# Optimization experiments

Measured on AMD Instinct MI355X. Metric: run time of the kernel, lower is better.

## Reference

```python
import jax, jax.numpy as jnp
import numpy as np

NUM_HEADS = 8
EMBED_DIM = 512


def _attention(q, k, v, mask=None):
    # q,k,v: [batch, heads, Lq, d] / [batch, heads, Lk, d]
    s = jnp.einsum('bhqd,bhkd->bhqk', q, k)
    if mask is not None:
        s = jnp.where(mask, jnp.asarray(-1000.0, s.dtype), s)
    p = jax.nn.softmax(s, axis=-1)
    return jnp.einsum('bhqk,bhkd->bhqd', p, v)


def _t_mask(T, H):
    # True where attention is DISALLOWED (query frame t_q < key frame t_k)
    tq = jnp.arange(T)[:, None]
    tk = jnp.arange(T)[None, :]
    blocked = tq < tk  # [T, T]
    m = jnp.repeat(jnp.repeat(blocked, H, axis=0), H, axis=1)  # [T*H, T*H]
    return m


def setup_inputs() -> dict:
    key = jax.random.key(0)
    ks = jax.random.split(key, 10)
    B, T, H, W, E = 4, 4, 28, 28, EMBED_DIM
    N = T * H * W
    s_in = (2.0 / (E + 3 * E)) ** 0.5  # xavier-ish
    s_sq = (1.0 / E) ** 0.5
    return {
        'x': jax.random.normal(ks[0], (B, N, E), dtype=jnp.float32),
        'in_proj_weight': jax.random.normal(ks[1], (3 * E, E), dtype=jnp.float32) * s_in,
        'in_proj_bias': jnp.zeros((3 * E,), dtype=jnp.float32),
        'out_proj_w': jax.random.normal(ks[2], (E, E), dtype=jnp.float32) * s_sq,
        'out_proj_b': jnp.zeros((E,), dtype=jnp.float32),
        'in_proj_weight_t': jax.random.normal(ks[3], (E, E), dtype=jnp.float32) * s_sq,
        'in_proj_bias_t': jnp.zeros((E,), dtype=jnp.float32),
        'out_proj_t_w': jax.random.normal(ks[4], (E, E), dtype=jnp.float32) * s_sq,
        'out_proj_t_b': jnp.zeros((E,), dtype=jnp.float32),
        'alpha': 0.0001 * jnp.ones((E,), dtype=jnp.float32),
        'H': 28,
        'W': 28,
    }


def reference(x, in_proj_weight, in_proj_bias, out_proj_w, out_proj_b,
              in_proj_weight_t, in_proj_bias_t, out_proj_t_w, out_proj_t_b,
              alpha, H, W):
    B, N, C = x.shape
    nh = NUM_HEADS
    hc = C // nh
    T = N // (H * W)
    scale = hc ** (-0.5)

    # ---- spatial (per-frame) attention: _forward_2d ----
    qkv = x @ in_proj_weight.T + in_proj_bias            # [B, N, 3C]
    qkv = qkv.reshape(B, T, H * W, 3, nh, hc)
    qkv = qkv.transpose(3, 0, 1, 4, 2, 5).reshape(3, B * T, nh, H * W, hc)
    q, k, v = qkv[0], qkv[1], qkv[2]
    o = _attention(q * scale, k, v)                       # [B*T, nh, HW, hc]
    xs = o.transpose(0, 2, 1, 3).reshape(B, N, C)
    xs = xs @ out_proj_w.T + out_proj_b

    ks = jax.lax.stop_gradient(k)                         # detached cache
    vs = jax.lax.stop_gradient(v)

    # ---- axial temporal attention ----
    q_t = (x @ in_proj_weight_t.T + in_proj_bias_t) * scale  # [B, N, C]
    q_t = q_t.reshape(B, T, H, W, nh, hc)
    q_th = q_t.transpose(0, 3, 4, 1, 2, 5).reshape(B * W, nh, T * H, hc)
    q_tw = q_t.transpose(0, 2, 4, 1, 3, 5).reshape(B * H, nh, T * W, hc)

    k6 = ks.reshape(B, T, nh, H, W, hc)
    v6 = vs.reshape(B, T, nh, H, W, hc)
    k_th = k6.transpose(0, 4, 2, 1, 3, 5).reshape(B * W, nh, T * H, hc)
    k_tw = k6.transpose(0, 3, 2, 1, 4, 5).reshape(B * H, nh, T * W, hc)
    v_th = v6.transpose(0, 4, 2, 1, 3, 5).reshape(B * W, nh, T * H, hc)
    v_tw = v6.transpose(0, 3, 2, 1, 4, 5).reshape(B * H, nh, T * W, hc)

    o_th = _attention(q_th, k_th, v_th, _t_mask(T, H))    # [B*W, nh, T*H, hc]
    o_tw = _attention(q_tw, k_tw, v_tw, _t_mask(T, W))    # [B*H, nh, T*W, hc]

    o_th = o_th.reshape(B, W, nh, T, H, hc).transpose(0, 3, 4, 1, 2, 5).reshape(B, N, C)
    o_tw = o_tw.reshape(B, H, nh, T, W, hc).transpose(0, 3, 1, 4, 2, 5).reshape(B, N, C)

    x_t = (o_th + o_tw) @ out_proj_t_w.T + out_proj_t_b
    return xs + alpha * x_t
```

## Files before the change

kernel.cpp:

```cpp
#include <hip/hip_runtime.h>
#include <stdint.h>

#define NN   3136
#define MM   12544
#define SCALE 0.125f
#define MASKED (-30000.0f)

typedef __attribute__((ext_vector_type(8))) unsigned short ushort8;
typedef __attribute__((ext_vector_type(8))) short short8;
typedef __attribute__((ext_vector_type(4))) float floatx4;

__device__ __forceinline__ float b2f(unsigned short u) {
    union { unsigned int i; float f; } x; x.i = ((unsigned int)u) << 16; return x.f;
}
__device__ __forceinline__ unsigned short f2b(float f) {
    union { float f; unsigned int i; } x; x.f = f;
    unsigned int r = x.i + 0x7fffu + ((x.i >> 16) & 1u);
    return (unsigned short)(r >> 16);
}
__device__ __forceinline__ void load8(const void* p, size_t e, int isf32, float o[8]) {
    if (isf32) {
        const float* f = (const float*)p + e;
        #pragma unroll
        for (int i = 0; i < 8; ++i) o[i] = f[i];
    } else {
        ushort8 u = *(const ushort8*)((const unsigned short*)p + e);
        #pragma unroll
        for (int i = 0; i < 8; ++i) o[i] = b2f(u[i]);
    }
}
__device__ __forceinline__ float load1(const void* p, int e, int isf32) {
    return isf32 ? ((const float*)p)[e] : b2f(((const unsigned short*)p)[e]);
}

__global__ void detect_dtype(const void* __restrict__ x, int* __restrict__ flagp)
{
    if (threadIdx.x == 0 && blockIdx.x == 0) {
        const unsigned short* u = (const unsigned short*)x;
        int c = 0;
        for (int i = 0; i < 512; ++i) {
            const float v = b2f(u[i]);
            if (!(v == v) || fabsf(v) > 1000.0f) ++c;
        }
        *flagp = (c >= 16) ? 1 : 0;
    }
}

__global__ __launch_bounds__(256) void convert_x(
    const int* __restrict__ flagp, const float* __restrict__ x,
    unsigned short* __restrict__ xb)
{
    if (!*flagp) return;
    const size_t i = ((size_t)blockIdx.x * 256 + threadIdx.x) * 8;
    const float4 a = *(const float4*)(x + i);
    const float4 b = *(const float4*)(x + i + 4);
    ushort8 o;
    o[0] = f2b(a.x); o[1] = f2b(a.y); o[2] = f2b(a.z); o[3] = f2b(a.w);
    o[4] = f2b(b.x); o[5] = f2b(b.y); o[6] = f2b(b.z); o[7] = f2b(b.w);
    *(ushort8*)(xb + i) = o;
}

__global__ __launch_bounds__(256) void gemm_proj_mfma(
    const int* __restrict__ flagp, const void* __restrict__ x,
    const unsigned short* __restrict__ xb,
    const void* __restrict__ Wi, const void* __restrict__ bi,
    const void* __restrict__ Wt, const void* __restrict__ bt,
    unsigned short* __restrict__ qkv, unsigned short* __restrict__ qt)
{
    __shared__ unsigned short A_sh[128][40];
    __shared__ unsigned short B_sh[64][40];
    const int gid = blockIdx.x;
    const int mt = (gid >> 8) * 8 + (gid & 7);
    const int nt = (gid & 255) >> 3;
    if (mt >= 98) return;
    const int m0 = mt * 128, n0 = nt * 64;

    const int isf32 = *flagp;
    const unsigned short* A = isf32 ? xb : (const unsigned short*)x;
    const int tid = threadIdx.x, lane = tid & 63, wv = tid >> 6;
    const int lane15 = lane & 15, quad = lane >> 4;
    const int wm = wv >> 1, wn = wv & 1;

    const int ra = tid >> 1, ca = (tid & 1) * 16;
    const int rb = tid >> 2, cb = (tid & 3) * 8;
    const int nb = n0 + rb;
    const bool isWt = (nb >= 1536);

    floatx4 acc[4][2];
    #pragma unroll
    for (int i = 0; i < 4; ++i)
        #pragma unroll
        for (int j = 0; j < 2; ++j) acc[i][j] = (floatx4){0.f,0.f,0.f,0.f};

    for (int k0 = 0; k0 < 512; k0 += 32) {
        const unsigned short* ap = A + (size_t)(m0 + ra) * 512 + k0 + ca;
        *(ushort8*)&A_sh[ra][ca]     = *(const ushort8*)ap;
        *(ushort8*)&A_sh[ra][ca + 8] = *(const ushort8*)(ap + 8);
        float wvv[8];
        if (!isWt) load8(Wi, (size_t)nb * 512 + k0 + cb, isf32, wvv);
        else {
            load8(Wt, (size_t)(nb - 1536) * 512 + k0 + cb, isf32, wvv);
            #pragma unroll
            for (int u = 0; u < 8; ++u) wvv[u] *= SCALE;
        }
        #pragma unroll
        for (int u = 0; u < 8; ++u) B_sh[rb][cb + u] = f2b(wvv[u]);
        __syncthreads();

        short8 af[4], bf[2];
        #pragma unroll
        for (int i = 0; i < 4; ++i)
            af[i] = *(const short8*)&A_sh[wm * 64 + i * 16 + lane15][quad * 8];
        #pragma unroll
        for (int j = 0; j < 2; ++j)
            bf[j] = *(const short8*)&B_sh[wn * 32 + j * 16 + lane15][quad * 8];
        #pragma unroll
        for (int i = 0; i < 4; ++i)
            #pragma unroll
            for (int j = 0; j < 2; ++j)
                acc[i][j] = __builtin_amdgcn_mfma_f32_16x16x32_bf16(af[i], bf[j], acc[i][j], 0, 0, 0);
        __syncthreads();
    }

    #pragma unroll
    for (int j = 0; j < 2; ++j) {
        const int col = n0 + wn * 32 + j * 16 + lane15;
        float bias;
        unsigned short* dst;
        int stride;
        if (col < 1536) { bias = load1(bi, col, isf32); dst = qkv; stride = 1536; }
        else { bias = SCALE * load1(bt, col - 1536, isf32); dst = qt; stride = 512; }
        const int cofs = (col < 1536) ? col : (col - 1536);
        #pragma unroll
        for (int i = 0; i < 4; ++i)
            #pragma unroll
            for (int r = 0; r < 4; ++r) {
                const int m = m0 + wm * 64 + i * 16 + quad * 4 + r;
                dst[(size_t)m * stride + cofs] = f2b(acc[i][j][r] + bias);
            }
    }
}

__global__ __launch_bounds__(256) void gemm_final_mfma(
    const int* __restrict__ flagp,
    const unsigned short* __restrict__ qkv, const unsigned short* __restrict__ qt,
    const void* __restrict__ Wo, const void* __restrict__ Wto,
    const void* __restrict__ bo, const void* __restrict__ bto,
    const void* __restrict__ alp, void* __restrict__ outp)
{
    __shared__ unsigned short A_sh[128][40];
    __shared__ unsigned short B_sh[64][40];
    const int gid = blockIdx.x;
    const int mt = (gid >> 6) * 8 + (gid & 7);
    const int nt = (gid & 63) >> 3;
    if (mt >= 98) return;
    const int m0 = mt * 128, n0 = nt * 64;

    const int isf32 = *flagp;
    const int tid = threadIdx.x, lane = tid & 63, wv = tid >> 6;
    const int lane15 = lane & 15, quad = lane >> 4;
    const int wm = wv >> 1, wn = wv & 1;

    const int ra = tid >> 1, ca = (tid & 1) * 16;
    const int rb = tid >> 2, cb = (tid & 3) * 8;
    const int nb = n0 + rb;
    const float al_b = load1(alp, nb, isf32);

    floatx4 acc[4][2];
    #pragma unroll
    for (int i = 0; i < 4; ++i)
        #pragma unroll
        for (int j = 0; j < 2; ++j) acc[i][j] = (floatx4){0.f,0.f,0.f,0.f};

    for (int k0 = 0; k0 < 1024; k0 += 32) {
        const int m = m0 + ra;
        const unsigned short* ap = (k0 < 512)
            ? qkv + (size_t)m * 1536 + k0 + ca
            : qt  + (size_t)m * 512  + (k0 - 512) + ca;
        *(ushort8*)&A_sh[ra][ca]     = *(const ushort8*)ap;
        *(ushort8*)&A_sh[ra][ca + 8] = *(const ushort8*)(ap + 8);
        float wvv[8];
        if (k0 < 512) load8(Wo, (size_t)nb * 512 + k0 + cb, isf32, wvv);
        else {
            load8(Wto, (size_t)nb * 512 + (k0 - 512) + cb, isf32, wvv);
            #pragma unroll
            for (int u = 0; u < 8; ++u) wvv[u] *= al_b;
        }
        #pragma unroll
        for (int u = 0; u < 8; ++u) B_sh[rb][cb + u] = f2b(wvv[u]);
        __syncthreads();

        short8 af[4], bf[2];
        #pragma unroll
        for (int i = 0; i < 4; ++i)
            af[i] = *(const short8*)&A_sh[wm * 64 + i * 16 + lane15][quad * 8];
        #pragma unroll
        for (int j = 0; j < 2; ++j)
            bf[j] = *(const short8*)&B_sh[wn * 32 + j * 16 + lane15][quad * 8];
        #pragma unroll
        for (int i = 0; i < 4; ++i)
            #pragma unroll
            for (int j = 0; j < 2; ++j)
                acc[i][j] = __builtin_amdgcn_mfma_f32_16x16x32_bf16(af[i], bf[j], acc[i][j], 0, 0, 0);
        __syncthreads();
    }

    #pragma unroll
    for (int j = 0; j < 2; ++j) {
        const int col = n0 + wn * 32 + j * 16 + lane15;
        const float bias = load1(bo, col, isf32) + load1(alp, col, isf32) * load1(bto, col, isf32);
        #pragma unroll
        for (int i = 0; i < 4; ++i)
            #pragma unroll
            for (int r = 0; r < 4; ++r) {
                const int m = m0 + wm * 64 + i * 16 + quad * 4 + r;
                const float val = acc[i][j][r] + bias;
                const size_t idx = (size_t)m * 512 + col;
                if (isf32) ((float*)outp)[idx] = val;
                else       ((unsigned short*)outp)[idx] = f2b(val);
            }
    }
}

__global__ __launch_bounds__(256) void attn_spatial_mfma(unsigned short* __restrict__ qkv)
{
    __shared__ unsigned short K_sh[64][72];
    __shared__ unsigned short VT_sh[64][72];
    __shared__ unsigned short P_sh[4][16][72];

    const int tid = threadIdx.x, lane = tid & 63, wv = tid >> 6;
    const int lane15 = lane & 15, quad = lane >> 4;
    const int qb = blockIdx.x, head = blockIdx.y, bt = blockIdx.z;
    const int qt_idx = qb * 4 + wv;
    const bool active = (qt_idx < 49);
    const int q0 = active ? qt_idx * 16 : 0;
    const int frame0 = bt * 784;

    short8 q_lo = {0,0,0,0,0,0,0,0}, q_hi = {0,0,0,0,0,0,0,0};
    if (active) {
        const unsigned short* qp = qkv + (size_t)(frame0 + q0 + lane15) * 1536 + head * 64 + quad * 8;
        q_lo = *(const short8*)qp;
        q_hi = *(const short8*)(qp + 32);
    }

    floatx4 accO[4] = {{0.f,0.f,0.f,0.f},{0.f,0.f,0.f,0.f},{0.f,0.f,0.f,0.f},{0.f,0.f,0.f,0.f}};
    float lsum[4] = {0.f, 0.f, 0.f, 0.f};

    const int r_st = tid >> 2, c_st = (tid & 3) << 4;

    for (int kt = 0; kt < 13; ++kt) {
        __syncthreads();
        ushort8 k8a = {0,0,0,0,0,0,0,0}, k8b = {0,0,0,0,0,0,0,0};
        ushort8 v8a = {0,0,0,0,0,0,0,0}, v8b = {0,0,0,0,0,0,0,0};
        const int key = kt * 64 + r_st;
        if (key < 784) {
            const unsigned short* kp = qkv + (size_t)(frame0 + key) * 1536 + head * 64 + c_st;
            k8a = *(const ushort8*)(kp + 512);
            k8b = *(const ushort8*)(kp + 520);
            v8a = *(const ushort8*)(kp + 1024);
            v8b = *(const ushort8*)(kp + 1032);
        }
        *(ushort8*)&K_sh[r_st][c_st]     = k8a;
        *(ushort8*)&K_sh[r_st][c_st + 8] = k8b;
        #pragma unroll
        for (int u = 0; u < 8; ++u) {
            VT_sh[c_st + u][r_st]     = v8a[u];
            VT_sh[c_st + 8 + u][r_st] = v8b[u];
        }
        __syncthreads();
        if (!active) continue;

        floatx4 s[4];
        #pragma unroll
        for (int st = 0; st < 4; ++st) {
            const short8 kfl = *(const short8*)&K_sh[st * 16 + lane15][quad * 8];
            const short8 kfh = *(const short8*)&K_sh[st * 16 + lane15][32 + quad * 8];
            floatx4 a = {0.f,0.f,0.f,0.f};
            a = __builtin_amdgcn_mfma_f32_16x16x32_bf16(q_lo, kfl, a, 0, 0, 0);
            a = __builtin_amdgcn_mfma_f32_16x16x32_bf16(q_hi, kfh, a, 0, 0, 0);
            s[st] = a;
        }

        const bool tail = (kt == 12);
        #pragma unroll
        for (int st = 0; st < 4; ++st)
            #pragma unroll
            for (int r = 0; r < 4; ++r) {
                const float v = (tail && st >= 1) ? MASKED : s[st][r] * SCALE;
                const float p = __expf(v);
                lsum[r] += p;
                P_sh[wv][quad * 4 + r][st * 16 + lane15] = f2b(p);
            }

        #pragma unroll
        for (int kc = 0; kc < 2; ++kc) {
            const short8 pf = *(const short8*)&P_sh[wv][lane15][kc * 32 + quad * 8];
            #pragma unroll
            for (int nt = 0; nt < 4; ++nt) {
                const short8 vf = *(const short8*)&VT_sh[nt * 16 + lane15][kc * 32 + quad * 8];
                accO[nt] = __builtin_amdgcn_mfma_f32_16x16x32_bf16(pf, vf, accO[nt], 0, 0, 0);
            }
        }
    }

    #pragma unroll
    for (int off = 1; off < 16; off <<= 1)
        #pragma unroll
        for (int r = 0; r < 4; ++r)
            lsum[r] += __shfl_xor(lsum[r], off, 64);

    if (active) {
        #pragma unroll
        for (int nt = 0; nt < 4; ++nt)
            #pragma unroll
            for (int r = 0; r < 4; ++r) {
                const int qrow = q0 + quad * 4 + r;
                qkv[(size_t)(frame0 + qrow) * 1536 + head * 64 + nt * 16 + lane15]
                    = f2b(accO[nt][r] / lsum[r]);
            }
    }
}

__global__ __launch_bounds__(256) void attn_axial(
    const unsigned short* __restrict__ qkv, const unsigned short* __restrict__ qtu,
    const unsigned short* __restrict__ oth, unsigned short* __restrict__ outp,
    const int pass)
{
    __shared__ unsigned short K_sh[112][72];
    __shared__ unsigned short VT_sh[64][136];
    __shared__ unsigned short P_sh[4][16][136];

    const int tid = threadIdx.x, lane = tid & 63, wv = tid >> 6;
    const int lane15 = lane & 15, quad = lane >> 4;
    const int b = blockIdx.x / 28, pos = blockIdx.x % 28;
    const int head = blockIdx.y;
    const int r_st = tid >> 3, c_st = (tid & 7) << 3;

    #pragma unroll
    for (int rnd = 0; rnd < 4; ++rnd) {
        const int j = rnd * 32 + r_st;
        if (j < 112) {
            const int tk = j / 28, rk = j % 28;
            const int n_k = tk * 784 + (pass == 0 ? rk * 28 + pos : pos * 28 + rk);
            const unsigned short* kp = qkv + (size_t)(b * NN + n_k) * 1536 + 512 + head * 64 + c_st;
            const ushort8 k8 = *(const ushort8*)kp;
            const ushort8 v8 = *(const ushort8*)(kp + 512);
            *(ushort8*)&K_sh[j][c_st] = k8;
            #pragma unroll
            for (int u = 0; u < 8; ++u) VT_sh[c_st + u][j] = v8[u];
        } else {
            #pragma unroll
            for (int u = 0; u < 8; ++u) VT_sh[c_st + u][j] = 0;
        }
    }
    __syncthreads();

    for (int tile = wv; tile < 7; tile += 4) {
        const int iq = tile * 16 + lane15;
        const int tq_q = iq / 28, rq = iq % 28;
        const int n_q = tq_q * 784 + (pass == 0 ? rq * 28 + pos : pos * 28 + rq);
        const size_t qaddr = (size_t)(b * NN + n_q) * 512 + head * 64;
        const short8 q_lo = *(const short8*)(qtu + qaddr + quad * 8);
        const short8 q_hi = *(const short8*)(qtu + qaddr + 32 + quad * 8);

        floatx4 s[7];
        #pragma unroll
        for (int st = 0; st < 7; ++st) {
            const short8 kfl = *(const short8*)&K_sh[st * 16 + lane15][quad * 8];
            const short8 kfh = *(const short8*)&K_sh[st * 16 + lane15][32 + quad * 8];
            floatx4 acc = {0.f,0.f,0.f,0.f};
            acc = __builtin_amdgcn_mfma_f32_16x16x32_bf16(q_lo, kfl, acc, 0, 0, 0);
            acc = __builtin_amdgcn_mfma_f32_16x16x32_bf16(q_hi, kfh, acc, 0, 0, 0);
            s[st] = acc;
        }

        int tq_row[4];
        #pragma unroll
        for (int r = 0; r < 4; ++r) tq_row[r] = (tile * 16 + quad * 4 + r) / 28;
        float l[4] = {0.f, 0.f, 0.f, 0.f};
        #pragma unroll
        for (int st = 0; st < 7; ++st) {
            const int tk = (st * 16 + lane15) / 28;
            #pragma unroll
            for (int r = 0; r < 4; ++r) {
                const float v = (tk <= tq_row[r]) ? s[st][r] : MASKED;
                const float p = __expf(v);
                s[st][r] = p;
                l[r] += p;
            }
        }
        #pragma unroll
        for (int off = 1; off < 16; off <<= 1)
            #pragma unroll
            for (int r = 0; r < 4; ++r)
                l[r] += __shfl_xor(l[r], off, 64);

        #pragma unroll
        for (int r = 0; r < 4; ++r) {
            const int row = quad * 4 + r;
            #pragma unroll
            for (int st = 0; st < 7; ++st)
                P_sh[wv][row][st * 16 + lane15] = f2b(s[st][r]);
            P_sh[wv][row][112 + lane15] = 0;
        }

        floatx4 accO[4] = {{0.f,0.f,0.f,0.f},{0.f,0.f,0.f,0.f},{0.f,0.f,0.f,0.f},{0.f,0.f,0.f,0.f}};
        #pragma unroll
        for (int kc = 0; kc < 4; ++kc) {
            const short8 pf = *(const short8*)&P_sh[wv][lane15][kc * 32 + quad * 8];
            #pragma unroll
            for (int nt = 0; nt < 4; ++nt) {
                const short8 vf = *(const short8*)&VT_sh[nt * 16 + lane15][kc * 32 + quad * 8];
                accO[nt] = __builtin_amdgcn_mfma_f32_16x16x32_bf16(pf, vf, accO[nt], 0, 0, 0);
            }
        }

        #pragma unroll
        for (int r = 0; r < 4; ++r) {
            const int io = tile * 16 + quad * 4 + r;
            const int to = io / 28, ro = io % 28;
            const int n_o = to * 784 + (pass == 0 ? ro * 28 + pos : pos * 28 + ro);
            const size_t oaddr = (size_t)(b * NN + n_o) * 512 + head * 64;
            #pragma unroll
            for (int nt = 0; nt < 4; ++nt) {
                float o = accO[nt][r] / l[r];
                if (pass == 1) o += b2f(oth[oaddr + nt * 16 + lane15]);
                outp[oaddr + nt * 16 + lane15] = f2b(o);
            }
        }
    }
}

__global__ void fill_val(unsigned short* o, unsigned short v, int n) {
    const int i = blockIdx.x * 256 + threadIdx.x;
    if (i < n) o[i] = v;
}

extern "C" void kernel_launch(void* const* d_in, const int* in_sizes, int n_in,
                              void* d_out, int out_size, void* d_ws, size_t ws_size,
                              hipStream_t stream)
{
    const void* x   = d_in[0];
    const void* Wi  = d_in[1];
    const void* bi  = d_in[2];
    const void* Wo  = d_in[3];
    const void* bo  = d_in[4];
    const void* Wt  = d_in[5];
    const void* bt  = d_in[6];
    const void* Wto = d_in[7];
    const void* bto = d_in[8];
    const void* alp = d_in[9];

    const size_t QKV_ELEMS = (size_t)MM * 1536;
    const size_t QT_ELEMS  = (size_t)MM * 512;
    const size_t FLAG_OFF  = (QKV_ELEMS + QT_ELEMS) * 2;
    const size_t NEED      = FLAG_OFF + 256;

    if (ws_size < NEED) {
        fill_val<<<dim3((out_size + 255) / 256), dim3(256), 0, stream>>>(
            (unsigned short*)d_out, (unsigned short)0x3f80, out_size);
        return;
    }

    unsigned short* qkv = (unsigned short*)d_ws;
    unsigned short* qt  = qkv + QKV_ELEMS;
    int* flagp = (int*)((char*)d_ws + FLAG_OFF);
    unsigned short* oth = (unsigned short*)d_out;
    unsigned short* xb  = oth + (size_t)MM * 512;

    dim3 blk(256);
    detect_dtype<<<dim3(1), dim3(64), 0, stream>>>(x, flagp);
    convert_x<<<dim3(MM * 512 / (256 * 8)), blk, 0, stream>>>(flagp, (const float*)x, xb);
    gemm_proj_mfma<<<dim3(13 * 256), blk, 0, stream>>>(
        flagp, x, xb, Wi, bi, Wt, bt, qkv, qt);
    attn_spatial_mfma<<<dim3(13, 8, 16), blk, 0, stream>>>(qkv);
    attn_axial<<<dim3(112, 8), blk, 0, stream>>>(qkv, qt, nullptr, oth, 0);
    attn_axial<<<dim3(112, 8), blk, 0, stream>>>(qkv, qt, oth, qt, 1);
    gemm_final_mfma<<<dim3(13 * 64), blk, 0, stream>>>(
        flagp, qkv, qt, Wo, Wto, bo, bto, alp, d_out);
}
```

Measured before the change: 331.0 us.

## Swizzle LDS layouts for V/P tiles and remap spatial blocks per XCD

XOR-swizzles the column index of the transposed V tile and the P tile in shared memory, in both the spatial and the axial attention kernels. The goal is to cut LDS bank conflicts on the scalar transposed stores and the vector fragment reads. The spatial kernel also switches to a 1D grid whose block IDs are remapped so that all query blocks of one (frame, head) group land on the same XCD, which should improve L2 reuse of that group's K/V. The swizzles must agree exactly between writers and readers, or outputs will be wrong.

```diff
diff --git a/kernel.cpp b/kernel.cpp
--- a/kernel.cpp
+++ b/kernel.cpp
@@ -230,7 +230,13 @@
 
     const int tid = threadIdx.x, lane = tid & 63, wv = tid >> 6;
     const int lane15 = lane & 15, quad = lane >> 4;
-    const int qb = blockIdx.x, head = blockIdx.y, bt = blockIdx.z;
+
+    const int gid = blockIdx.x;
+    const int xcd = gid & 7, kk = gid >> 3;
+    const int grp = xcd * 16 + kk / 13;
+    const int qb  = kk % 13;
+    const int head = grp & 7, bt = grp >> 3;
+
     const int qt_idx = qb * 4 + wv;
     const bool active = (qt_idx < 49);
     const int q0 = active ? qt_idx * 16 : 0;
@@ -247,6 +253,8 @@
     float lsum[4] = {0.f, 0.f, 0.f, 0.f};
 
     const int r_st = tid >> 2, c_st = (tid & 3) << 4;
+    const int swzv = c_st;
+    const int swzp = (lane15 >> 2) << 4;
 
     for (int kt = 0; kt < 13; ++kt) {
         __syncthreads();
@@ -264,8 +272,8 @@
         *(ushort8*)&K_sh[r_st][c_st + 8] = k8b;
         #pragma unroll
         for (int u = 0; u < 8; ++u) {
-            VT_sh[c_st + u][r_st]     = v8a[u];
-            VT_sh[c_st + 8 + u][r_st] = v8b[u];
+            VT_sh[c_st + u][r_st ^ swzv]     = v8a[u];
+            VT_sh[c_st + 8 + u][r_st ^ swzv] = v8b[u];
         }
         __syncthreads();
         if (!active) continue;
@@ -289,15 +297,15 @@
                 const float v = (tail && st >= 1) ? MASKED : s[st][r] * SCALE;
                 const float p = __expf(v);
                 lsum[r] += p;
-                P_sh[wv][quad * 4 + r][st * 16 + lane15] = f2b(p);
+                P_sh[wv][quad * 4 + r][(st * 16 + lane15) ^ (quad << 4)] = f2b(p);
             }
 
         #pragma unroll
         for (int kc = 0; kc < 2; ++kc) {
-            const short8 pf = *(const short8*)&P_sh[wv][lane15][kc * 32 + quad * 8];
+            const short8 pf = *(const short8*)&P_sh[wv][lane15][(kc * 32 + quad * 8) ^ swzp];
             #pragma unroll
             for (int nt = 0; nt < 4; ++nt) {
-                const short8 vf = *(const short8*)&VT_sh[nt * 16 + lane15][kc * 32 + quad * 8];
+                const short8 vf = *(const short8*)&VT_sh[nt * 16 + lane15][(kc * 32 + quad * 8) ^ (nt << 4)];
                 accO[nt] = __builtin_amdgcn_mfma_f32_16x16x32_bf16(pf, vf, accO[nt], 0, 0, 0);
             }
         }
@@ -335,6 +343,7 @@
     const int b = blockIdx.x / 28, pos = blockIdx.x % 28;
     const int head = blockIdx.y;
     const int r_st = tid >> 3, c_st = (tid & 7) << 3;
+    const int swzp = (lane15 >> 2) << 4;
 
     #pragma unroll
     for (int rnd = 0; rnd < 4; ++rnd) {
@@ -347,10 +356,10 @@
             const ushort8 v8 = *(const ushort8*)(kp + 512);
             *(ushort8*)&K_sh[j][c_st] = k8;
             #pragma unroll
-            for (int u = 0; u < 8; ++u) VT_sh[c_st + u][j] = v8[u];
+            for (int u = 0; u < 8; ++u) VT_sh[c_st + u][j ^ c_st] = v8[u];
         } else {
             #pragma unroll
-            for (int u = 0; u < 8; ++u) VT_sh[c_st + u][j] = 0;
+            for (int u = 0; u < 8; ++u) VT_sh[c_st + u][j ^ c_st] = 0;
         }
     }
     __syncthreads();
@@ -400,17 +409,18 @@
             const int row = quad * 4 + r;
             #pragma unroll
             for (int st = 0; st < 7; ++st)
-                P_sh[wv][row][st * 16 + lane15] = f2b(s[st][r]);
-            P_sh[wv][row][112 + lane15] = 0;
+                P_sh[wv][row][(st * 16 + lane15) ^ (quad << 4)] = f2b(s[st][r]);
+            P_sh[wv][row][(112 + lane15) ^ (quad << 4)] = 0;
         }
 
         floatx4 accO[4] = {{0.f,0.f,0.f,0.f},{0.f,0.f,0.f,0.f},{0.f,0.f,0.f,0.f},{0.f,0.f,0.f,0.f}};
         #pragma unroll
         for (int kc = 0; kc < 4; ++kc) {
-            const short8 pf = *(const short8*)&P_sh[wv][lane15][kc * 32 + quad * 8];
+            const short8 pf = *(const short8*)&P_sh[wv][lane15][(kc * 32 + quad * 8) ^ swzp];
             #pragma unroll
             for (int nt = 0; nt < 4; ++nt) {
-                const short8 vf = *(const short8*)&VT_sh[nt * 16 + lane15][kc * 32 + quad * 8];
+                const int row = nt * 16 + lane15;
+                const short8 vf = *(const short8*)&VT_sh[row][(kc * 32 + quad * 8) ^ ((row >> 3) << 3)];
                 accO[nt] = __builtin_amdgcn_mfma_f32_16x16x32_bf16(pf, vf, accO[nt], 0, 0, 0);
             }
         }
@@ -473,7 +483,7 @@
     convert_x<<<dim3(MM * 512 / (256 * 8)), blk, 0, stream>>>(flagp, (const float*)x, xb);
     gemm_proj_mfma<<<dim3(13 * 256), blk, 0, stream>>>(
         flagp, x, xb, Wi, bi, Wt, bt, qkv, qt);
-    attn_spatial_mfma<<<dim3(13, 8, 16), blk, 0, stream>>>(qkv);
+    attn_spatial_mfma<<<dim3(13 * 128), blk, 0, stream>>>(qkv);
     attn_axial<<<dim3(112, 8), blk, 0, stream>>>(qkv, qt, nullptr, oth, 0);
     attn_axial<<<dim3(112, 8), blk, 0, stream>>>(qkv, qt, oth, qt, 1);
     gemm_final_mfma<<<dim3(13 * 64), blk, 0, stream>>>(
```

Result: faster. 322.3 us (-2.6%).
